# Kernel tuning notes

Measured on AMD Instinct MI355X. Metric: run time of the kernel, lower is better.

## Reference

```python
import jax, jax.numpy as jnp
import numpy as np

DIM = 512
HEADS = 8
HEAD_DIM = DIM // HEADS
B, N = 4, 8192


def setup_inputs() -> dict:
    key = jax.random.key(0)
    k1, k2, k3, k4 = jax.random.split(key, 4)
    x = jax.random.normal(k1, (B, N, DIM), dtype=jnp.float32)
    # torch Linear weight is [out, in]; store transposed [in, out] for x @ W
    Wqkv = jax.random.normal(k2, (DIM, 3 * DIM), dtype=jnp.float32) * (DIM ** -0.5)
    Wout = jax.random.normal(k3, (DIM, DIM), dtype=jnp.float32) * (DIM ** -0.5)
    bout = jax.random.normal(k4, (DIM,), dtype=jnp.float32) * 0.01
    return {"x": x, "Wqkv": Wqkv, "Wout": Wout, "bout": bout}


def reference(x, Wqkv, Wout, bout):
    b, n, d = x.shape
    h, hd = HEADS, HEAD_DIM
    qkv = x @ Wqkv  # [b, n, 3d]
    q, k, v = jnp.split(qkv, 3, axis=-1)
    # [b, n, d] -> [b, h, n, hd]
    def to_heads(t):
        return t.reshape(b, n, h, hd).transpose(0, 2, 1, 3)
    q, k, v = to_heads(q), to_heads(k), to_heads(v)
    q = jax.nn.elu(q) + 1.0
    k = jax.nn.elu(k) + 1.0
    kv = jnp.einsum('bhnd,bhne->bhde', k, v)          # [b,h,hd,hd]
    z = 1.0 / (jnp.einsum('bhnd,bhd->bhn', q, k.sum(axis=2)) + 1e-6)
    out = jnp.einsum('bhnd,bhde->bhne', q, kv) * z[..., None]
    out = out.transpose(0, 2, 1, 3).reshape(b, n, d)
    # dropout in eval mode is identity
    return out @ Wout + bout
```

## Files before the change

kernel.cpp:

```cpp
#include <hip/hip_runtime.h>

typedef unsigned short u16;
typedef __bf16 bf16x8 __attribute__((ext_vector_type(8)));
typedef float f32x4 __attribute__((ext_vector_type(4)));

#define DEV static __device__ __forceinline__

DEV float bf2f(u16 u) { unsigned x = ((unsigned)u) << 16; return __builtin_bit_cast(float, x); }
DEV u16 f2bf(float f) {
  unsigned u = __builtin_bit_cast(unsigned, f);
  u += 0x7FFFu + ((u >> 16) & 1u);
  return (u16)(u >> 16);
}
DEV int swz(int b) { return b ^ ((((b >> 7) & 7)) << 4); }

#define GLD_LDS16(gp, lp)                                                    \
  __builtin_amdgcn_global_load_lds(                                          \
      (__attribute__((address_space(1))) void*)(void*)(gp),                  \
      (__attribute__((address_space(3))) void*)(lp), 16, 0, 0)

#define BAR() __builtin_amdgcn_s_barrier()
#define WAIT_LGKM0()                                                         \
  { asm volatile("s_waitcnt lgkmcnt(0)" ::: "memory");                       \
    __builtin_amdgcn_sched_barrier(0); }
#define WAIT_VM(n) asm volatile("s_waitcnt vmcnt(" #n ")" ::: "memory")

__global__ __launch_bounds__(256) void convert_bf16_kernel(
    const float* __restrict__ in, u16* __restrict__ out) {
  const size_t i = (size_t)blockIdx.x * 256 + threadIdx.x;
  const float4* p = (const float4*)in + 2 * i;
  float4 a = p[0], b = p[1];
  unsigned w0 = (unsigned)f2bf(a.x) | ((unsigned)f2bf(a.y) << 16);
  unsigned w1 = (unsigned)f2bf(a.z) | ((unsigned)f2bf(a.w) << 16);
  unsigned w2 = (unsigned)f2bf(b.x) | ((unsigned)f2bf(b.y) << 16);
  unsigned w3 = (unsigned)f2bf(b.z) | ((unsigned)f2bf(b.w) << 16);
  ((uint4*)out)[i] = make_uint4(w0, w1, w2, w3);
}

__global__ void transpose_bf16(const float* __restrict__ W, u16* __restrict__ Wt,
                               int K, int Ncols) {
  __shared__ float t[32][33];
  const int tx = threadIdx.x & 31, ty = threadIdx.x >> 5;
  const int n0 = blockIdx.x * 32, k0 = blockIdx.y * 32;
#pragma unroll
  for (int i = 0; i < 4; ++i)
    t[ty + i * 8][tx] = W[(size_t)(k0 + ty + i * 8) * Ncols + n0 + tx];
  __syncthreads();
#pragma unroll
  for (int i = 0; i < 4; ++i)
    Wt[(size_t)(n0 + ty + i * 8) * K + k0 + tx] = f2bf(t[tx][ty + i * 8]);
}

template <int MODE>
__global__ __launch_bounds__(512, 2) void gemm8_kernel(
    const u16* __restrict__ A, const u16* __restrict__ Bt,
    u16* __restrict__ qb, u16* __restrict__ kb, u16* __restrict__ vb,
    float* __restrict__ Cf, const float* __restrict__ bias) {
  constexpr int NX = (MODE == 0) ? 6 : 2;
  constexpr int K = 512;
  __shared__ __align__(16) u16 As[2][2][8192];
  __shared__ __align__(16) u16 Bs[2][2][8192];

  const int tid = threadIdx.x;
  const int lane = tid & 63;
  const int wid = tid >> 6;
  const int wr = wid >> 2;
  const int wcn = wid & 3;

  const int nwg = gridDim.x;
  const int pb = blockIdx.x;
  const int logical = (pb & 7) * (nwg >> 3) + (pb >> 3);
  const int rowBase = (logical / NX) * 256;
  const int colBase = (logical % NX) * 256;

  int soff[2], od[2];
#pragma unroll
  for (int i = 0; i < 2; ++i) {
    int o = (wid * 2 + i) * 1024 + lane * 16;
    int a = o ^ (((o >> 7) & 7) << 4);
    soff[i] = (a >> 7) * K + ((a & 127) >> 1);
    od[i] = (wid * 2 + i) * 512;
  }
  const u16* Abase = A + (size_t)rowBase * K;
  const u16* Bbase = Bt + (size_t)colBase * K;

#define STAGE_A(tau, h)                                                      \
  { const u16* g = Abase + (size_t)(h)*128 * K + (tau)*64;                   \
    _Pragma("unroll") for (int i = 0; i < 2; ++i)                            \
        GLD_LDS16(g + soff[i], &As[(tau)&1][h][od[i]]); }
#define STAGE_B(tau, h)                                                      \
  { const u16* g = Bbase + (size_t)(h)*128 * K + (tau)*64;                   \
    _Pragma("unroll") for (int i = 0; i < 2; ++i)                            \
        GLD_LDS16(g + soff[i], &Bs[(tau)&1][h][od[i]]); }

  const int sx = (lane & 7) << 4;
  int rb[2];
#pragma unroll
  for (int ks = 0; ks < 2; ++ks)
    rb[ks] = ((lane & 15) * 128 + ks * 64 + (lane >> 4) * 16) ^ sx;
  const char* Ahalf[2] = {(const char*)&As[0][wr][0], (const char*)&As[1][wr][0]};
  const char* Bhalf[2] = {(const char*)&Bs[0][wcn >> 1][0], (const char*)&Bs[1][wcn >> 1][0]};

  bf16x8 aA[4][2], bB0[2][2], bB1[2][2];
  f32x4 acc[8][4];
  f32x4 zv = {0.f, 0.f, 0.f, 0.f};
#pragma unroll
  for (int m = 0; m < 8; ++m)
#pragma unroll
    for (int n = 0; n < 4; ++n) acc[m][n] = zv;

#define LDA_FRAGS(par, mh)                                                   \
  _Pragma("unroll") for (int m = 0; m < 4; ++m)                              \
      _Pragma("unroll") for (int ks = 0; ks < 2; ++ks)                       \
          aA[m][ks] = *(const bf16x8*)(Ahalf[par] + (mh)*8192 + m * 2048 + rb[ks]);
#define LDB_FRAGS(par, nh, dst)                                              \
  _Pragma("unroll") for (int n = 0; n < 2; ++n)                              \
      _Pragma("unroll") for (int ks = 0; ks < 2; ++ks)                       \
          dst[n][ks] = *(const bf16x8*)(Bhalf[par] + (wcn & 1) * 8192 +      \
                                        (nh)*4096 + n * 2048 + rb[ks]);
#define MFMA_QUAD(mh, nh, bsrc)                                              \
  __builtin_amdgcn_s_setprio(1);                                             \
  _Pragma("unroll") for (int m = 0; m < 4; ++m)                              \
      _Pragma("unroll") for (int n = 0; n < 2; ++n)                          \
          _Pragma("unroll") for (int ks = 0; ks < 2; ++ks)                   \
              acc[(mh)*4 + m][(nh)*2 + n] =                                  \
                  __builtin_amdgcn_mfma_f32_16x16x32_bf16(                   \
                      aA[m][ks], bsrc[n][ks], acc[(mh)*4 + m][(nh)*2 + n],   \
                      0, 0, 0);                                              \
  __builtin_amdgcn_s_setprio(0);

  STAGE_A(0, 0); STAGE_A(0, 1); STAGE_B(0, 0); STAGE_B(0, 1);
  STAGE_B(1, 0); STAGE_A(1, 0);
  WAIT_VM(4);
  BAR();

  for (int t = 0; t < 6; t += 2) {
    LDA_FRAGS(0, 0); LDB_FRAGS(0, 0, bB0);
    STAGE_B(t + 1, 1);
    BAR(); WAIT_LGKM0();
    MFMA_QUAD(0, 0, bB0);
    BAR();
    LDB_FRAGS(0, 1, bB1);
    STAGE_A(t + 1, 1);
    BAR(); WAIT_LGKM0();
    MFMA_QUAD(0, 1, bB1);
    BAR();
    LDA_FRAGS(0, 1);
    STAGE_B(t + 2, 0);
    BAR(); WAIT_LGKM0();
    MFMA_QUAD(1, 1, bB1);
    BAR();
    STAGE_A(t + 2, 0);
    BAR(); WAIT_LGKM0();
    MFMA_QUAD(1, 0, bB0);
    WAIT_VM(4);
    BAR();
    LDA_FRAGS(1, 0); LDB_FRAGS(1, 0, bB0);
    STAGE_A(t + 2, 1);
    BAR(); WAIT_LGKM0();
    MFMA_QUAD(0, 0, bB0);
    BAR();
    LDB_FRAGS(1, 1, bB1);
    STAGE_B(t + 2, 1);
    BAR(); WAIT_LGKM0();
    MFMA_QUAD(0, 1, bB1);
    BAR();
    LDA_FRAGS(1, 1);
    STAGE_B(t + 3, 0);
    BAR(); WAIT_LGKM0();
    MFMA_QUAD(1, 1, bB1);
    BAR();
    STAGE_A(t + 3, 0);
    BAR(); WAIT_LGKM0();
    MFMA_QUAD(1, 0, bB0);
    WAIT_VM(4);
    BAR();
  }

  LDA_FRAGS(0, 0); LDB_FRAGS(0, 0, bB0);
  STAGE_B(7, 1);
  BAR(); WAIT_LGKM0();
  MFMA_QUAD(0, 0, bB0);
  BAR();
  LDB_FRAGS(0, 1, bB1);
  STAGE_A(7, 1);
  BAR(); WAIT_LGKM0();
  MFMA_QUAD(0, 1, bB1);
  BAR();
  LDA_FRAGS(0, 1);
  BAR(); WAIT_LGKM0();
  MFMA_QUAD(1, 1, bB1);
  BAR();
  BAR(); WAIT_LGKM0();
  MFMA_QUAD(1, 0, bB0);
  WAIT_VM(0);
  BAR();
  LDA_FRAGS(1, 0); LDB_FRAGS(1, 0, bB0);
  BAR(); WAIT_LGKM0();
  MFMA_QUAD(0, 0, bB0);
  BAR();
  LDB_FRAGS(1, 1, bB1);
  BAR(); WAIT_LGKM0();
  MFMA_QUAD(0, 1, bB1);
  BAR();
  LDA_FRAGS(1, 1);
  BAR(); WAIT_LGKM0();
  MFMA_QUAD(1, 1, bB1);
  BAR();
  BAR(); WAIT_LGKM0();
  MFMA_QUAD(1, 0, bB0);

  if (MODE == 0) {
    u16* dst = (colBase < 512) ? qb : (colBase < 1024) ? kb : vb;
    const int cb2 = colBase & 511;
    const bool doelu = (colBase < 1024);
    const int rbBase = (rowBase >> 4) + wr * 8;
    const int cbBase = (cb2 >> 4) + wcn * 4;
#pragma unroll
    for (int mi = 0; mi < 8; ++mi) {
#pragma unroll
      for (int ni = 0; ni < 4; ++ni) {
        float v[4];
#pragma unroll
        for (int r = 0; r < 4; ++r) {
          float t2 = acc[mi][ni][r];
          v[r] = doelu ? ((t2 > 0.f) ? t2 + 1.f : __expf(t2)) : t2;
        }
        unsigned lo = (unsigned)f2bf(v[0]) | ((unsigned)f2bf(v[1]) << 16);
        unsigned hi = (unsigned)f2bf(v[2]) | ((unsigned)f2bf(v[3]) << 16);
        size_t base = (((size_t)(rbBase + mi) * 32 + (cbBase + ni)) * 64 + lane) * 4;
        *(uint2*)(dst + base) = make_uint2(lo, hi);
      }
    }
  } else {
#pragma unroll
    for (int mi = 0; mi < 8; ++mi) {
#pragma unroll
      for (int ni = 0; ni < 4; ++ni) {
        const int col = colBase + wcn * 64 + ni * 16 + (lane & 15);
#pragma unroll
        for (int r = 0; r < 4; ++r) {
          const int row = rowBase + wr * 128 + mi * 16 + (lane >> 4) * 4 + r;
          Cf[(size_t)row * 512 + col] = acc[mi][ni][r] + bias[col];
        }
      }
    }
  }
#undef STAGE_A
#undef STAGE_B
#undef LDA_FRAGS
#undef LDB_FRAGS
#undef MFMA_QUAD
}

__global__ __launch_bounds__(256, 2) void kv_partial_kernel(
    const u16* __restrict__ kb, const u16* __restrict__ vb,
    float* __restrict__ part) {
  __shared__ float kf[128][64];
  __shared__ float vf[128][64];
  const int tid = threadIdx.x;
  const int chunk = blockIdx.x;
  const int bh = blockIdx.y;
  const int b = bh >> 3, h = bh & 7;
  const size_t rbase = (size_t)b * 8192;
  const int hcb = h * 4;
  const int dg = tid >> 4, eg = tid & 15;

  float acc[4][4] = {};
  float ks[4] = {};

  for (int st = 0; st < 4; ++st) {
    const int n0 = chunk * 512 + st * 128;
    const int rbT = (int)((rbase + n0) >> 4);
#pragma unroll
    for (int it = 0; it < 4; ++it) {
      int flat = it * 256 + tid;
      int frag = flat >> 5, w = flat & 31;
      int rb_i = frag >> 2, cb_i = frag & 3;
      size_t src = (((size_t)(rbT + rb_i) * 32 + hcb + cb_i) * 64 + w * 2) * 4;
      uint4 kraw = *(const uint4*)(kb + src);
      uint4 vraw = *(const uint4*)(vb + src);
      int l0 = w * 2;
      int row0 = rb_i * 16 + ((l0 >> 4) << 2);
      int col0 = cb_i * 16 + (l0 & 15);
      *(float2*)&kf[row0 + 0][col0] = make_float2(bf2f((u16)(kraw.x & 0xFFFF)), bf2f((u16)(kraw.z & 0xFFFF)));
      *(float2*)&kf[row0 + 1][col0] = make_float2(bf2f((u16)(kraw.x >> 16)), bf2f((u16)(kraw.z >> 16)));
      *(float2*)&kf[row0 + 2][col0] = make_float2(bf2f((u16)(kraw.y & 0xFFFF)), bf2f((u16)(kraw.w & 0xFFFF)));
      *(float2*)&kf[row0 + 3][col0] = make_float2(bf2f((u16)(kraw.y >> 16)), bf2f((u16)(kraw.w >> 16)));
      *(float2*)&vf[row0 + 0][col0] = make_float2(bf2f((u16)(vraw.x & 0xFFFF)), bf2f((u16)(vraw.z & 0xFFFF)));
      *(float2*)&vf[row0 + 1][col0] = make_float2(bf2f((u16)(vraw.x >> 16)), bf2f((u16)(vraw.z >> 16)));
      *(float2*)&vf[row0 + 2][col0] = make_float2(bf2f((u16)(vraw.y & 0xFFFF)), bf2f((u16)(vraw.w & 0xFFFF)));
      *(float2*)&vf[row0 + 3][col0] = make_float2(bf2f((u16)(vraw.y >> 16)), bf2f((u16)(vraw.w >> 16)));
    }
    __syncthreads();
#pragma unroll 4
    for (int n = 0; n < 128; ++n) {
      float4 kk = *(const float4*)&kf[n][dg * 4];
      float4 vv = *(const float4*)&vf[n][eg * 4];
      float ka[4] = {kk.x, kk.y, kk.z, kk.w};
      float va[4] = {vv.x, vv.y, vv.z, vv.w};
#pragma unroll
      for (int i = 0; i < 4; ++i)
#pragma unroll
        for (int j = 0; j < 4; ++j) acc[i][j] += ka[i] * va[j];
      if (eg == 0) {
#pragma unroll
        for (int i = 0; i < 4; ++i) ks[i] += ka[i];
      }
    }
    __syncthreads();
  }

  float* pp = part + ((size_t)bh * 16 + chunk) * (64 * 80);
#pragma unroll
  for (int i = 0; i < 4; ++i) {
#pragma unroll
    for (int j = 0; j < 4; ++j) pp[(dg * 4 + i) * 80 + eg * 4 + j] = acc[i][j];
    if (eg == 0) pp[(dg * 4 + i) * 80 + 64] = ks[i];
  }
}

__global__ void kv_reduce_kernel(const float* __restrict__ part,
                                 float* __restrict__ kv_ext) {
  const int idx = blockIdx.x * 256 + threadIdx.x;
  const int bh = idx / 5120;
  const int de = idx % 5120;
  const int e = de % 80;
  float s = 0.f;
  if (e <= 64) {
    for (int c = 0; c < 16; ++c) s += part[((size_t)bh * 16 + c) * 5120 + de];
  }
  kv_ext[idx] = s;
}

__global__ __launch_bounds__(256, 2) void attn_kernel(
    const u16* __restrict__ qb, const float* __restrict__ kv_ext,
    u16* __restrict__ attn) {
  __shared__ __align__(16) float kvs[64 * 80];
  __shared__ __align__(16) u16 qs[4][64 * 64];
  const int tid = threadIdx.x, lane = tid & 63, wid = tid >> 6;
  const int nchunk = blockIdx.x, bh = blockIdx.y;
  const int b = bh >> 3, h = bh & 7;

#pragma unroll
  for (int i = 0; i < 20; ++i)
    kvs[i * 256 + tid] = kv_ext[(size_t)bh * 5120 + i * 256 + tid];
  __syncthreads();

  bf16x8 bfr[5][2];
#pragma unroll
  for (int eb = 0; eb < 5; ++eb)
#pragma unroll
    for (int ksi = 0; ksi < 2; ++ksi) {
      unsigned pw[4];
#pragma unroll
      for (int jj = 0; jj < 4; ++jj) {
        int d0 = ksi * 32 + (lane >> 4) * 8 + 2 * jj;
        int e = eb * 16 + (lane & 15);
        unsigned lo = f2bf(kvs[d0 * 80 + e]);
        unsigned hi = f2bf(kvs[(d0 + 1) * 80 + e]);
        pw[jj] = lo | (hi << 16);
      }
      uint4 u = make_uint4(pw[0], pw[1], pw[2], pw[3]);
      bfr[eb][ksi] = __builtin_bit_cast(bf16x8, u);
    }

  const size_t row0 = (size_t)b * 8192 + (size_t)nchunk * 256 + wid * 64;
  const int rbQ = (int)(row0 >> 4);
  const int hcbQ = h * 4;
  char* qsw = (char*)&qs[wid][0];
#pragma unroll
  for (int it = 0; it < 8; ++it) {
    int flat = it * 64 + lane;
    int frag = flat >> 5, w = flat & 31;
    int rb_i = frag >> 2, cb_i = frag & 3;
    size_t src = (((size_t)(rbQ + rb_i) * 32 + hcbQ + cb_i) * 64 + w * 2) * 4;
    uint4 q4 = *(const uint4*)(qb + src);
    int l0 = w * 2;
    int row = rb_i * 16 + ((l0 >> 4) << 2);
    int col = cb_i * 16 + (l0 & 15);
    int bb = row * 128 + col * 2;
    *(unsigned*)(qsw + swz(bb)) = (q4.x & 0xFFFF) | ((q4.z & 0xFFFF) << 16);
    *(unsigned*)(qsw + swz(bb + 128)) = (q4.x >> 16) | (q4.z & 0xFFFF0000u);
    *(unsigned*)(qsw + swz(bb + 256)) = (q4.y & 0xFFFF) | ((q4.w & 0xFFFF) << 16);
    *(unsigned*)(qsw + swz(bb + 384)) = (q4.y >> 16) | (q4.w & 0xFFFF0000u);
  }
  WAIT_LGKM0();

  f32x4 zv = {0.f, 0.f, 0.f, 0.f};
  f32x4 acc[4][5];
#pragma unroll
  for (int m = 0; m < 4; ++m)
#pragma unroll
    for (int eb = 0; eb < 5; ++eb) acc[m][eb] = zv;

#pragma unroll
  for (int m = 0; m < 4; ++m)
#pragma unroll
    for (int ksi = 0; ksi < 2; ++ksi) {
      int bb = (m * 16 + (lane & 15)) * 128 + (ksi * 32 + (lane >> 4) * 8) * 2;
      bf16x8 af = *(const bf16x8*)(qsw + swz(bb));
#pragma unroll
      for (int eb = 0; eb < 5; ++eb)
        acc[m][eb] = __builtin_amdgcn_mfma_f32_16x16x32_bf16(af, bfr[eb][ksi], acc[m][eb], 0, 0, 0);
    }

#pragma unroll
  for (int m = 0; m < 4; ++m) {
#pragma unroll
    for (int r = 0; r < 4; ++r) {
      float den = __shfl(acc[m][4][r], lane & ~15, 64);
      float zr = 1.f / (den + 1e-6f);
      int row = m * 16 + (lane >> 4) * 4 + r;
#pragma unroll
      for (int eb = 0; eb < 4; ++eb) {
        int col = eb * 16 + (lane & 15);
        *(u16*)(qsw + swz(row * 128 + col * 2)) = f2bf(acc[m][eb][r] * zr);
      }
    }
  }
  WAIT_LGKM0();
#pragma unroll
  for (int jt = 0; jt < 8; ++jt) {
    int flat = jt * 64 + lane;
    int row = flat >> 3, w = flat & 7;
    uint4 val = *(const uint4*)(qsw + swz(row * 128 + w * 16));
    *(uint4*)(attn + (row0 + row) * 512 + h * 64 + w * 8) = val;
  }
}

extern "C" void kernel_launch(void* const* d_in, const int* in_sizes, int n_in,
                              void* d_out, int out_size, void* d_ws, size_t ws_size,
                              hipStream_t stream) {
  const float* x = (const float*)d_in[0];
  const float* Wqkv = (const float*)d_in[1];
  const float* Wout = (const float*)d_in[2];
  const float* bout = (const float*)d_in[3];
  float* out = (float*)d_out;

  char* ws = (char*)d_ws;
  u16* qb = (u16*)ws;        ws += (size_t)32768 * 512 * 2;
  u16* kb = (u16*)ws;        ws += (size_t)32768 * 512 * 2;
  u16* vb = (u16*)ws;        ws += (size_t)32768 * 512 * 2;
  u16* wqkv_t = (u16*)ws;    ws += (size_t)1536 * 512 * 2;
  u16* wout_t = (u16*)ws;    ws += (size_t)512 * 512 * 2;
  float* kv_ext = (float*)ws; ws += (size_t)32 * 64 * 80 * 4;
  float* part = (float*)ws;   ws += (size_t)32 * 16 * 64 * 80 * 4;

  u16* xb = (u16*)d_out;

  convert_bf16_kernel<<<8192, 256, 0, stream>>>(x, xb);
  transpose_bf16<<<dim3(1536 / 32, 512 / 32), 256, 0, stream>>>(Wqkv, wqkv_t, 512, 1536);
  transpose_bf16<<<dim3(512 / 32, 512 / 32), 256, 0, stream>>>(Wout, wout_t, 512, 512);
  gemm8_kernel<0><<<768, 512, 0, stream>>>(xb, wqkv_t, qb, kb, vb, nullptr, nullptr);
  kv_partial_kernel<<<dim3(16, 32), 256, 0, stream>>>(kb, vb, part);
  kv_reduce_kernel<<<640, 256, 0, stream>>>(part, kv_ext);
  attn_kernel<<<dim3(32, 32), 256, 0, stream>>>(qb, kv_ext, vb);
  gemm8_kernel<1><<<256, 512, 0, stream>>>(vb, wout_t, nullptr, nullptr, nullptr, out, bout);
}
```

Before: 170.0 us.

## Compute K^T V partials with bf16 MFMA and register-prefetched loads

Replaces the scalar FP32 outer-product kv_partial kernel with an MFMA version. Each wave transposes its K/V tiles into swizzled LDS, accumulates K^T V plus the key sum (using an all-ones B operand) on 16x16x32 bf16 MFMAs, and prefetches the next tile into registers while computing. Per-wave accumulators are reduced in LDS, and the chunk count is halved to 8, which shrinks the partial buffer and the reduce loop. The cost is 80KB of LDS per block, which limits occupancy, and only 256 blocks are launched.

```diff
diff --git a/kernel.cpp b/kernel.cpp
--- a/kernel.cpp
+++ b/kernel.cpp
@@ -253,71 +253,114 @@
 #undef MFMA_QUAD
 }
 
-__global__ __launch_bounds__(256, 2) void kv_partial_kernel(
+__global__ __launch_bounds__(256, 2) void kv_partial_mfma(
     const u16* __restrict__ kb, const u16* __restrict__ vb,
     float* __restrict__ part) {
-  __shared__ float kf[128][64];
-  __shared__ float vf[128][64];
-  const int tid = threadIdx.x;
+  __shared__ __align__(16) char lds[81920];
+  const int tid = threadIdx.x, lane = tid & 63, wid = tid >> 6;
   const int chunk = blockIdx.x;
   const int bh = blockIdx.y;
   const int b = bh >> 3, h = bh & 7;
-  const size_t rbase = (size_t)b * 8192;
   const int hcb = h * 4;
-  const int dg = tid >> 4, eg = tid & 15;
-
-  float acc[4][4] = {};
-  float ks[4] = {};
-
-  for (int st = 0; st < 4; ++st) {
-    const int n0 = chunk * 512 + st * 128;
-    const int rbT = (int)((rbase + n0) >> 4);
-#pragma unroll
-    for (int it = 0; it < 4; ++it) {
-      int flat = it * 256 + tid;
-      int frag = flat >> 5, w = flat & 31;
-      int rb_i = frag >> 2, cb_i = frag & 3;
-      size_t src = (((size_t)(rbT + rb_i) * 32 + hcb + cb_i) * 64 + w * 2) * 4;
-      uint4 kraw = *(const uint4*)(kb + src);
-      uint4 vraw = *(const uint4*)(vb + src);
-      int l0 = w * 2;
-      int row0 = rb_i * 16 + ((l0 >> 4) << 2);
-      int col0 = cb_i * 16 + (l0 & 15);
-      *(float2*)&kf[row0 + 0][col0] = make_float2(bf2f((u16)(kraw.x & 0xFFFF)), bf2f((u16)(kraw.z & 0xFFFF)));
-      *(float2*)&kf[row0 + 1][col0] = make_float2(bf2f((u16)(kraw.x >> 16)), bf2f((u16)(kraw.z >> 16)));
-      *(float2*)&kf[row0 + 2][col0] = make_float2(bf2f((u16)(kraw.y & 0xFFFF)), bf2f((u16)(kraw.w & 0xFFFF)));
-      *(float2*)&kf[row0 + 3][col0] = make_float2(bf2f((u16)(kraw.y >> 16)), bf2f((u16)(kraw.w >> 16)));
-      *(float2*)&vf[row0 + 0][col0] = make_float2(bf2f((u16)(vraw.x & 0xFFFF)), bf2f((u16)(vraw.z & 0xFFFF)));
-      *(float2*)&vf[row0 + 1][col0] = make_float2(bf2f((u16)(vraw.x >> 16)), bf2f((u16)(vraw.z >> 16)));
-      *(float2*)&vf[row0 + 2][col0] = make_float2(bf2f((u16)(vraw.y & 0xFFFF)), bf2f((u16)(vraw.w & 0xFFFF)));
-      *(float2*)&vf[row0 + 3][col0] = make_float2(bf2f((u16)(vraw.y >> 16)), bf2f((u16)(vraw.w >> 16)));
-    }
-    __syncthreads();
-#pragma unroll 4
-    for (int n = 0; n < 128; ++n) {
-      float4 kk = *(const float4*)&kf[n][dg * 4];
-      float4 vv = *(const float4*)&vf[n][eg * 4];
-      float ka[4] = {kk.x, kk.y, kk.z, kk.w};
-      float va[4] = {vv.x, vv.y, vv.z, vv.w};
-#pragma unroll
-      for (int i = 0; i < 4; ++i)
-#pragma unroll
-        for (int j = 0; j < 4; ++j) acc[i][j] += ka[i] * va[j];
-      if (eg == 0) {
-#pragma unroll
-        for (int i = 0; i < 4; ++i) ks[i] += ka[i];
+
+  char* kTc = lds + wid * 16384;
+  char* vTc = kTc + 8192;
+  const int rb0 = b * 512 + chunk * 64 + wid * 16;
+
+  uint4 kreg[8], vreg[8];
+
+#define KV_LOAD(it)                                                          \
+  _Pragma("unroll") for (int q = 0; q < 8; ++q) {                            \
+    int u = q * 64 + lane;                                                   \
+    int fid = u >> 5, w = u & 31;                                            \
+    int rbl = fid >> 2, cbi = fid & 3;                                       \
+    size_t fb = ((size_t)(rb0 + (it)*4 + rbl) * 32 + hcb + cbi) * 32 + w;    \
+    kreg[q] = ((const uint4*)kb)[fb];                                        \
+    vreg[q] = ((const uint4*)vb)[fb];                                        \
+  }
+
+#define KV_WRITE()                                                           \
+  _Pragma("unroll") for (int q = 0; q < 8; ++q) {                            \
+    int u = q * 64 + lane;                                                   \
+    int fid = u >> 5, w = u & 31;                                            \
+    int rbl = fid >> 2, cbi = fid & 3;                                       \
+    int l0 = 2 * w;                                                          \
+    int d0 = cbi * 16 + (l0 & 15);                                           \
+    int n0 = rbl * 16 + (l0 >> 4) * 4;                                       \
+    int a0 = swz(d0 * 128 + n0 * 2);                                         \
+    int a1 = swz((d0 + 1) * 128 + n0 * 2);                                   \
+    *(uint2*)(kTc + a0) = make_uint2(kreg[q].x, kreg[q].y);                  \
+    *(uint2*)(kTc + a1) = make_uint2(kreg[q].z, kreg[q].w);                  \
+    *(uint2*)(vTc + a0) = make_uint2(vreg[q].x, vreg[q].y);                  \
+    *(uint2*)(vTc + a1) = make_uint2(vreg[q].z, vreg[q].w);                  \
+  }
+
+  const uint4 onesu = make_uint4(0x3F803F80u, 0x3F803F80u, 0x3F803F80u, 0x3F803F80u);
+  const bf16x8 ones = __builtin_bit_cast(bf16x8, onesu);
+
+  f32x4 zv = {0.f, 0.f, 0.f, 0.f};
+  f32x4 acc[4][5];
+#pragma unroll
+  for (int mb = 0; mb < 4; ++mb)
+#pragma unroll
+    for (int eb = 0; eb < 5; ++eb) acc[mb][eb] = zv;
+
+  KV_LOAD(0);
+#pragma unroll
+  for (int it = 0; it < 4; ++it) {
+    WAIT_VM(0);
+    KV_WRITE();
+    if (it < 3) KV_LOAD(it + 1);
+    WAIT_LGKM0();
+#pragma unroll
+    for (int ks = 0; ks < 2; ++ks) {
+      bf16x8 afr[4], bvf[4];
+#pragma unroll
+      for (int mb = 0; mb < 4; ++mb)
+        afr[mb] = *(const bf16x8*)(kTc + swz((mb * 16 + (lane & 15)) * 128 +
+                                             (ks * 32 + (lane >> 4) * 8) * 2));
+#pragma unroll
+      for (int eb = 0; eb < 4; ++eb)
+        bvf[eb] = *(const bf16x8*)(vTc + swz((eb * 16 + (lane & 15)) * 128 +
+                                             (ks * 32 + (lane >> 4) * 8) * 2));
+      WAIT_LGKM0();
+#pragma unroll
+      for (int mb = 0; mb < 4; ++mb) {
+#pragma unroll
+        for (int eb = 0; eb < 4; ++eb)
+          acc[mb][eb] = __builtin_amdgcn_mfma_f32_16x16x32_bf16(
+              afr[mb], bvf[eb], acc[mb][eb], 0, 0, 0);
+        acc[mb][4] = __builtin_amdgcn_mfma_f32_16x16x32_bf16(
+            afr[mb], ones, acc[mb][4], 0, 0, 0);
       }
     }
-    __syncthreads();
-  }
-
-  float* pp = part + ((size_t)bh * 16 + chunk) * (64 * 80);
-#pragma unroll
-  for (int i = 0; i < 4; ++i) {
-#pragma unroll
-    for (int j = 0; j < 4; ++j) pp[(dg * 4 + i) * 80 + eg * 4 + j] = acc[i][j];
-    if (eg == 0) pp[(dg * 4 + i) * 80 + 64] = ks[i];
-  }
+  }
+
+  __syncthreads();
+  float* red = (float*)lds;
+#pragma unroll
+  for (int mb = 0; mb < 4; ++mb)
+#pragma unroll
+    for (int eb = 0; eb < 5; ++eb)
+      ((f32x4*)red)[wid * 1280 + (mb * 5 + eb) * 64 + lane] = acc[mb][eb];
+  __syncthreads();
+
+  float* pp = part + ((size_t)bh * 8 + chunk) * 5120;
+  const int lane_s = tid >> 2, r = tid & 3;
+#pragma unroll
+  for (int fi = 0; fi < 20; ++fi) {
+    float s = red[fi * 256 + tid] + red[5120 + fi * 256 + tid] +
+              red[10240 + fi * 256 + tid] + red[15360 + fi * 256 + tid];
+    const int mb = fi / 5, eb = fi % 5;
+    const int d = mb * 16 + (lane_s >> 4) * 4 + r;
+    if (eb < 4) {
+      pp[d * 80 + eb * 16 + (lane_s & 15)] = s;
+    } else if ((lane_s & 15) == 0) {
+      pp[d * 80 + 64] = s;
+    }
+  }
+#undef KV_LOAD
+#undef KV_WRITE
 }
 
 __global__ void kv_reduce_kernel(const float* __restrict__ part,
@@ -328,7 +371,7 @@
   const int e = de % 80;
   float s = 0.f;
   if (e <= 64) {
-    for (int c = 0; c < 16; ++c) s += part[((size_t)bh * 16 + c) * 5120 + de];
+    for (int c = 0; c < 8; ++c) s += part[((size_t)bh * 8 + c) * 5120 + de];
   }
   kv_ext[idx] = s;
 }
@@ -445,7 +488,7 @@
   u16* wqkv_t = (u16*)ws;    ws += (size_t)1536 * 512 * 2;
   u16* wout_t = (u16*)ws;    ws += (size_t)512 * 512 * 2;
   float* kv_ext = (float*)ws; ws += (size_t)32 * 64 * 80 * 4;
-  float* part = (float*)ws;   ws += (size_t)32 * 16 * 64 * 80 * 4;
+  float* part = (float*)ws;   ws += (size_t)32 * 8 * 64 * 80 * 4;
 
   u16* xb = (u16*)d_out;
 
@@ -453,7 +496,7 @@
   transpose_bf16<<<dim3(1536 / 32, 512 / 32), 256, 0, stream>>>(Wqkv, wqkv_t, 512, 1536);
   transpose_bf16<<<dim3(512 / 32, 512 / 32), 256, 0, stream>>>(Wout, wout_t, 512, 512);
   gemm8_kernel<0><<<768, 512, 0, stream>>>(xb, wqkv_t, qb, kb, vb, nullptr, nullptr);
-  kv_partial_kernel<<<dim3(16, 32), 256, 0, stream>>>(kb, vb, part);
+  kv_partial_mfma<<<dim3(8, 32), 256, 0, stream>>>(kb, vb, part);
   kv_reduce_kernel<<<640, 256, 0, stream>>>(part, kv_ext);
   attn_kernel<<<dim3(32, 32), 256, 0, stream>>>(qb, kv_ext, vb);
   gemm8_kernel<1><<<256, 512, 0, stream>>>(vb, wout_t, nullptr, nullptr, nullptr, out, bout);
```

Result: faster. 144.5 us (-15.0%).
